# Kernel tuning notes

Hardware: AMD Instinct MI355X
Metric: run time of the kernel (lower is better)

The kernel has to match this reference:

```python
import jax, jax.numpy as jnp
import numpy as np

ANG = 5
WS = 8
HEADS = 2
REF = 2  # refPos = [2, 2]
NEG_SLOPE = 0.1
EPS = 1e-5


def _rel_pos_index(ws):
    coords = np.stack(np.meshgrid(np.arange(ws), np.arange(ws), indexing='ij'))  # [2,ws,ws]
    cf = coords.reshape(2, -1)
    rel = (cf[:, :, None] - cf[:, None, :]).transpose(1, 2, 0)  # [N,N,2]
    rel[..., 0] += ws - 1
    rel[..., 1] += ws - 1
    rel[..., 0] *= 2 * ws - 1
    return jnp.asarray(rel.sum(-1))  # [N,N] int

REL_IDX = _rel_pos_index(WS)


def _ln(x, g, b):
    m = jnp.mean(x, -1, keepdims=True)
    v = jnp.var(x, -1, keepdims=True)
    return (x - m) * jax.lax.rsqrt(v + EPS) * g + b


def setup_inputs():
    key = jax.random.key(0)
    ks = jax.random.split(key, 12)
    b, an2, c, h, w = 2, 25, 32, 96, 96
    C = 2 * c
    s = 0.02
    mlp_hidden = int(C * 4.0)
    inp = {}
    inp['global_fea'] = jax.random.normal(ks[0], (b, an2, c, h, w), jnp.float32)
    inp['centra_fea'] = jax.random.normal(ks[1], (b, c, h, w), jnp.float32)
    inp['disparity'] = jax.random.uniform(ks[2], (b, 1, h, w), jnp.float32)
    inp['qkv_w'] = jax.random.normal(ks[3], (3 * C, C), jnp.float32) * s
    inp['qkv_b'] = jnp.zeros((3 * C,), jnp.float32)
    inp['proj_w'] = jax.random.normal(ks[4], (C, C), jnp.float32) * s
    inp['proj_b'] = jnp.zeros((C,), jnp.float32)
    inp['rpb_table'] = jax.random.normal(ks[5], ((2 * WS - 1) ** 2, HEADS), jnp.float32) * s
    inp['ln1_g'] = jnp.ones((C,), jnp.float32)
    inp['ln1_b'] = jnp.zeros((C,), jnp.float32)
    inp['ln2_g'] = jnp.ones((C,), jnp.float32)
    inp['ln2_b'] = jnp.zeros((C,), jnp.float32)
    inp['fc1_w'] = jax.random.normal(ks[6], (mlp_hidden, C), jnp.float32) * s
    inp['fc1_b'] = jnp.zeros((mlp_hidden,), jnp.float32)
    inp['fc2_w'] = jax.random.normal(ks[7], (C, mlp_hidden), jnp.float32) * s
    inp['fc2_b'] = jnp.zeros((C,), jnp.float32)
    inp['conv_w'] = jax.random.normal(ks[8], (c, C), jnp.float32) * s  # 1x1 conv kernel squeezed
    inp['conv_b'] = jnp.zeros((c,), jnp.float32)
    return inp


def _warp(centra_fea, disparity):
    # back-projection: bilinear warp of the central (2,2) view to all ANG*ANG views
    b, c, h, w = centra_fea.shape
    d = disparity[:, 0]  # [b,h,w]
    ys, xs = jnp.meshgrid(jnp.arange(h, dtype=jnp.float32), jnp.arange(w, dtype=jnp.float32), indexing='ij')
    offs = jnp.asarray([[u - REF, v - REF] for u in range(ANG) for v in range(ANG)], jnp.float32)  # [an2,2]
    sy = ys[None, None] + d[:, None] * offs[None, :, 0, None, None]  # [b,an2,h,w]
    sx = xs[None, None] + d[:, None] * offs[None, :, 1, None, None]
    x0f = jnp.floor(sx)
    y0f = jnp.floor(sy)
    wx = sx - x0f
    wy = sy - y0f
    x0 = jnp.clip(x0f.astype(jnp.int32), 0, w - 1)
    x1 = jnp.clip(x0 + 1, 0, w - 1)
    y0 = jnp.clip(y0f.astype(jnp.int32), 0, h - 1)
    y1 = jnp.clip(y0 + 1, 0, h - 1)
    flat = centra_fea.reshape(b, c, h * w)
    an2 = ANG * ANG

    def gather(yi, xi):
        idx = (yi * w + xi).reshape(b, 1, -1)  # [b,1,an2*h*w]
        g = jnp.take_along_axis(flat, jnp.broadcast_to(idx, (b, c, an2 * h * w)), axis=2)
        return g.reshape(b, c, an2, h, w).transpose(0, 2, 1, 3, 4)  # [b,an2,c,h,w]

    wx_ = wx[:, :, None]
    wy_ = wy[:, :, None]
    return ((1 - wy_) * (1 - wx_) * gather(y0, x0) + (1 - wy_) * wx_ * gather(y0, x1)
            + wy_ * (1 - wx_) * gather(y1, x0) + wy_ * wx_ * gather(y1, x1))


def reference(global_fea, centra_fea, disparity, qkv_w, qkv_b, proj_w, proj_b, rpb_table,
              ln1_g, ln1_b, ln2_g, ln2_b, fc1_w, fc1_b, fc2_w, fc2_b, conv_w, conv_b):
    b, an2, c, h, w = global_fea.shape
    warped = _warp(centra_fea, disparity)
    x = jnp.concatenate([global_fea, warped], axis=2)  # [b,an2,2c,h,w]
    C = 2 * c
    B = b * an2
    # 'b an2 c h w -> (b an2) (h w) c'
    x = x.reshape(B, C, h, w).transpose(0, 2, 3, 1).reshape(B, h * w, C)
    # --- Swin transformer block (shift_size=0, iteration_idx=0) ---
    shortcut = x
    xn = _ln(x, ln1_g, ln1_b).reshape(B, h, w, C)
    nh, nw = h // WS, w // WS
    xw = xn.reshape(B, nh, WS, nw, WS, C).transpose(0, 1, 3, 2, 4, 5).reshape(B * nh * nw, WS * WS, C)
    nwins, N = xw.shape[0], WS * WS
    hd = C // HEADS
    qkv = (xw @ qkv_w.T + qkv_b).reshape(nwins, N, 3, HEADS, hd).transpose(2, 0, 3, 1, 4)
    q, k, v = qkv[0], qkv[1], qkv[2]  # [nwins, heads, N, hd]
    scale = hd ** -0.5
    attn = jnp.einsum('whnd,whmd->whnm', q * scale, k)
    bias = rpb_table[REL_IDX].transpose(2, 0, 1)  # [heads,N,N]
    attn = jax.nn.softmax(attn + bias[None], axis=-1)
    out = jnp.einsum('whnm,whmd->whnd', attn, v).transpose(0, 2, 1, 3).reshape(nwins, N, C)
    out = out @ proj_w.T + proj_b
    out = out.reshape(B, nh, nw, WS, WS, C).transpose(0, 1, 3, 2, 4, 5).reshape(B, h * w, C)
    x = shortcut + out
    xm = _ln(x, ln2_g, ln2_b)
    xm = jax.nn.gelu(xm @ fc1_w.T + fc1_b, approximate=False) @ fc2_w.T + fc2_b
    x = x + xm
    # '(b an2) (h w) c -> (b an2) c h w' then 1x1 conv fuse + LeakyReLU(0.1)
    x = x.reshape(B, h, w, C)
    y = jnp.einsum('bhwc,oc->bohw', x, conv_w) + conv_b[None, :, None, None]
    y = jnp.where(y >= 0, y, NEG_SLOPE * y)
    return y.reshape(b, an2, c, h, w)
```

## Files before the change

### kernel.cpp

```cpp
#include <hip/hip_runtime.h>
#include <hip/hip_bf16.h>
#include <math.h>

#define W_    96
#define HW_   9216
#define NWIN_ 144

typedef __attribute__((ext_vector_type(4))) float          f32x4;
typedef __attribute__((ext_vector_type(8))) __bf16         bf16x8;
typedef __attribute__((ext_vector_type(8))) unsigned short u16x8;

#define MFMA(a,b,c) __builtin_amdgcn_mfma_f32_16x16x32_bf16((a),(b),(c),0,0,0)

#define WOFF_QKV  0
#define WOFF_PROJ 12288
#define WOFF_FC1  16384
#define WOFF_FC2  32768
#define WOFF_CONV 49152
#define WOFF_BIAS 51200
#define WTOT      51200
#define BIAS_N    8192
#define POFF_QKVB  0
#define POFF_PROJB 192
#define POFF_FC1B  256
#define POFF_FC2B  512
#define POFF_CONVB 576
#define POFF_RPB   608
#define POFF_LN1G  1058
#define POFF_LN1B  1122
#define POFF_LN2G  1186
#define POFF_LN2B  1250
#define PTOT       1314

__device__ __forceinline__ float ldin(const void* p, long i, int isbf){
    return isbf ? __bfloat162float(((const __hip_bfloat16*)p)[i]) : ((const float*)p)[i];
}
__device__ __forceinline__ bf16x8 ldbf8(const __bf16* w){
    u16x8 u = *(const u16x8*)w;
    return __builtin_bit_cast(bf16x8, u);
}

__device__ __forceinline__ float gelu_f(float v){
    float u = fabsf(v) * 0.70710678f;
    float t = __builtin_amdgcn_rcpf(1.f + 0.47047f*u);
    float p = t*(0.3480242f + t*(-0.0958798f + t*0.7478556f));
    float er = 1.f - p*__expf(-u*u);
    er = copysignf(er, v);
    return 0.5f*v*(1.f + er);
}

__global__ void probe_kernel(const void* ln1g, int* flag){
    if (threadIdx.x == 0){
        unsigned u = *(const unsigned*)ln1g;
        *flag = (u == 0x3F803F80u) ? 1 : 0;
    }
}

__global__ __launch_bounds__(256) void convert_params(
    const int* __restrict__ flag,
    const void* qkvw, const void* qkvb, const void* projw, const void* projb, const void* rpb,
    const void* ln1g, const void* ln1b, const void* ln2g, const void* ln2b,
    const void* fc1w, const void* fc1b, const void* fc2w, const void* fc2b,
    const void* convw, const void* convb,
    __bf16* __restrict__ wbf, float* __restrict__ pf)
{
    const int isbf = *flag;
    int idx = blockIdx.x*256 + threadIdx.x;
    if (idx >= WTOT + PTOT + BIAS_N) return;
    if (idx < WTOT){
        if      (idx < 12288) wbf[WOFF_QKV  + idx]          = (__bf16)ldin(qkvw, idx, isbf);
        else if (idx < 16384) wbf[WOFF_PROJ + (idx-12288)]  = (__bf16)ldin(projw, idx-12288, isbf);
        else if (idx < 32768) wbf[WOFF_FC1  + (idx-16384)]  = (__bf16)ldin(fc1w, idx-16384, isbf);
        else if (idx < 49152) wbf[WOFF_FC2  + (idx-32768)]  = (__bf16)ldin(fc2w, idx-32768, isbf);
        else                  wbf[WOFF_CONV + (idx-49152)]  = (__bf16)ldin(convw, idx-49152, isbf);
    } else if (idx < WTOT + PTOT){
        int p = idx - WTOT;
        if      (p < 192)  pf[POFF_QKVB  + p]        = ldin(qkvb, p, isbf);
        else if (p < 256)  pf[POFF_PROJB + (p-192)]  = ldin(projb, p-192, isbf);
        else if (p < 512)  pf[POFF_FC1B  + (p-256)]  = ldin(fc1b, p-256, isbf);
        else if (p < 576)  pf[POFF_FC2B  + (p-512)]  = ldin(fc2b, p-512, isbf);
        else if (p < 608)  pf[POFF_CONVB + (p-576)]  = ldin(convb, p-576, isbf);
        else if (p < 1058) pf[POFF_RPB   + (p-608)]  = ldin(rpb, p-608, isbf);
        else if (p < 1122) pf[POFF_LN1G  + (p-1058)] = ldin(ln1g, p-1058, isbf);
        else if (p < 1186) pf[POFF_LN1B  + (p-1122)] = ldin(ln1b, p-1122, isbf);
        else if (p < 1250) pf[POFF_LN2G  + (p-1186)] = ldin(ln2g, p-1186, isbf);
        else               pf[POFF_LN2B  + (p-1250)] = ldin(ln2b, p-1250, isbf);
    } else {
        int eb = idx - (WTOT + PTOT);
        int h = eb >> 12, rem = eb & 4095;
        int i = rem >> 6, j = rem & 63;
        int di = (i>>3)-(j>>3)+7, dj = (i&7)-(j&7)+7;
        wbf[WOFF_BIAS + eb] = (__bf16)ldin(rpb, (di*15+dj)*2 + h, isbf);
    }
}

template<typename T>
__device__ __forceinline__ void phaseA0(
    const T* gf, const T* disp,
    float* tile, int* iy0,int* iy1,int* ix0,int* ix1,float* fys,float* fxs,
    int tid,int b,int a,int wy,int wx,int hw00)
{
    if (tid < 64){
        int ty = tid >> 3, tx = tid & 7;
        int y = wy*8 + ty, x = wx*8 + tx;
        int pix = y*W_ + x;
        float d = (float)disp[(long)b*HW_ + pix];
        float dy = (float)(a/5 - 2), dx = (float)(a%5 - 2);
        float sy = (float)y + d*dy, sx = (float)x + d*dx;
        float y0f = floorf(sy), x0f = floorf(sx);
        fys[tid] = sy - y0f; fxs[tid] = sx - x0f;
        int y0 = min(max((int)y0f,0), W_-1);
        int x0 = min(max((int)x0f,0), W_-1);
        iy0[tid]=y0; iy1[tid]=min(y0+1,W_-1);
        ix0[tid]=x0; ix1[tid]=min(x0+1,W_-1);
    }
    int p = tid & 63;
    long pixoff = hw00 + (p>>3)*W_ + (p&7);
    for (int c = tid>>6; c < 32; c += 4)
        tile[c*67 + p] = (float)gf[(((long)b*25 + a)*32 + c)*HW_ + pixoff];
}

template<typename T>
__device__ __forceinline__ void phaseA1(
    const T* cf, float* tile2,
    const int* iy0,const int* iy1,const int* ix0,const int* ix1,const float* fys,const float* fxs,
    int tid,int b)
{
    int p = tid & 63;
    float fy = fys[p], fx = fxs[p];
    float w00=(1.f-fy)*(1.f-fx), w01=(1.f-fy)*fx, w10=fy*(1.f-fx), w11=fy*fx;
    long r0 = (long)iy0[p]*W_, r1 = (long)iy1[p]*W_;
    int xa = ix0[p], xb = ix1[p];
    for (int c = tid>>6; c < 32; c += 4){
        long cb = ((long)b*32 + c)*HW_;
        float v00 = (float)cf[cb+r0+xa], v01 = (float)cf[cb+r0+xb];
        float v10 = (float)cf[cb+r1+xa], v11 = (float)cf[cb+r1+xb];
        tile2[c*67 + p] = w00*v00 + w01*v01 + w10*v10 + w11*v11;
    }
}

__global__ __launch_bounds__(256) void fused_kernel(
    const int* __restrict__ flag,
    const void* __restrict__ gf, const void* __restrict__ cf, const void* __restrict__ disp,
    const __bf16* __restrict__ wbf, const float* __restrict__ pf,
    void* __restrict__ out)
{
    __shared__ __bf16 xs[64*72];
    __shared__ __bf16 arena[14336];

    const int isbf = *flag;
    const int tid  = threadIdx.x;
    const int lane = tid & 63, wid = tid >> 6;
    const int g = lane >> 4, cl = lane & 15;
    const int bid  = blockIdx.x;
    const int blk  = (bid & 7)*900 + (bid >> 3);
    const int Bidx = blk / NWIN_;
    const int wrem = blk % NWIN_;
    const int wy = wrem / 12, wx = wrem % 12;
    const int b = Bidx / 25, a = Bidx % 25;
    const int hw00 = (wy*8)*W_ + wx*8;

    __bf16* qb  = arena;
    __bf16* kb  = arena + 4608;
    __bf16* vT  = arena + 9216;
    __bf16* xn  = arena + 9728;

    float* tile  = (float*)arena;
    float* tile2 = tile + 2144;
    int*   iy0 = (int*)((char*)arena + 17408);
    int*   iy1 = iy0 + 64;
    int*   ix0 = iy1 + 64;
    int*   ix1 = ix0 + 64;
    float* fys = (float*)(ix1 + 64);
    float* fxs = fys + 64;

    if (isbf) phaseA0((const __hip_bfloat16*)gf, (const __hip_bfloat16*)disp,
                      tile, iy0,iy1,ix0,ix1,fys,fxs, tid,b,a,wy,wx,hw00);
    else      phaseA0((const float*)gf, (const float*)disp,
                      tile, iy0,iy1,ix0,ix1,fys,fxs, tid,b,a,wy,wx,hw00);
    __syncthreads();
    if (isbf) phaseA1((const __hip_bfloat16*)cf, tile2, iy0,iy1,ix0,ix1,fys,fxs, tid,b);
    else      phaseA1((const float*)cf, tile2, iy0,iy1,ix0,ix1,fys,fxs, tid,b);
    __syncthreads();

    {
        const int t = tid>>2, quad = tid&3;
        float v[16]; float sum=0.f, sq=0.f;
        #pragma unroll
        for (int j=0;j<16;++j){
            int c = quad*16+j;
            float val = (c<32) ? tile[c*67 + t] : tile2[(c-32)*67 + t];
            v[j]=val; sum+=val; sq+=val*val;
        }
        sum += __shfl_xor(sum,1); sq += __shfl_xor(sq,1);
        sum += __shfl_xor(sum,2); sq += __shfl_xor(sq,2);
        float m  = sum*(1.f/64.f);
        float rs = rsqrtf(sq*(1.f/64.f) - m*m + 1e-5f);
        bf16x8 s0,s1,n0,n1;
        #pragma unroll
        for (int j=0;j<8;++j){
            int c0 = quad*16+j, c1 = quad*16+8+j;
            s0[j] = (__bf16)v[j];
            s1[j] = (__bf16)v[8+j];
            n0[j] = (__bf16)((v[j]  -m)*rs*pf[POFF_LN1G+c0] + pf[POFF_LN1B+c0]);
            n1[j] = (__bf16)((v[8+j]-m)*rs*pf[POFF_LN1G+c1] + pf[POFF_LN1B+c1]);
        }
        *(bf16x8*)(xs + t*72 + quad*16)     = s0;
        *(bf16x8*)(xs + t*72 + quad*16 + 8) = s1;
        *(bf16x8*)(xn + t*72 + quad*16)     = n0;
        *(bf16x8*)(xn + t*72 + quad*16 + 8) = n1;
    }
    __syncthreads();

    {
        bf16x8 af[4][2];
        #pragma unroll
        for (int m=0;m<4;++m)
            #pragma unroll
            for (int ks=0;ks<2;++ks)
                af[m][ks] = *(const bf16x8*)(xn + (16*m+cl)*72 + ks*32 + 8*g);
        __syncthreads();
        f32x4 acc[3][4];
        #pragma unroll
        for (int nt=0;nt<3;++nt)
            #pragma unroll
            for (int m=0;m<4;++m) acc[nt][m] = (f32x4){0.f,0.f,0.f,0.f};
        const int f = wid*16 + cl;
        #pragma unroll
        for (int ks=0;ks<2;++ks)
            #pragma unroll
            for (int nt=0;nt<3;++nt){
                bf16x8 bw = ldbf8(wbf + WOFF_QKV + (long)(nt*64 + f)*64 + ks*32 + 8*g);
                #pragma unroll
                for (int m=0;m<4;++m) acc[nt][m] = MFMA(af[m][ks], bw, acc[nt][m]);
            }
        float bq = pf[POFF_QKVB + f], bk2 = pf[POFF_QKVB + 64 + f], bv2 = pf[POFF_QKVB + 128 + f];
        #pragma unroll
        for (int m=0;m<4;++m)
            #pragma unroll
            for (int r=0;r<4;++r){
                int t = 16*m + 4*g + r;
                qb[t*72 + f] = (__bf16)((acc[0][m][r] + bq)*0.1767766953f);
                kb[t*72 + f] = (__bf16)(acc[1][m][r] + bk2);
                vT[f*72 + t] = (__bf16)(acc[2][m][r] + bv2);
            }
    }
    __syncthreads();

    const int strip = wid*16;
    f32x4 sc[2][4];
    {
        bf16x8 aq0 = *(const bf16x8*)(qb + (strip+cl)*72 + 8*g);
        bf16x8 aq1 = *(const bf16x8*)(qb + (strip+cl)*72 + 32 + 8*g);
        #pragma unroll
        for (int h=0;h<2;++h)
            #pragma unroll
            for (int jt=0;jt<4;++jt){
                bf16x8 bk = *(const bf16x8*)(kb + (jt*16+cl)*72 + 32*h + 8*g);
                f32x4 z = {0.f,0.f,0.f,0.f};
                sc[h][jt] = MFMA(h?aq1:aq0, bk, z);
            }
        const __bf16* bptr = wbf + WOFF_BIAS + (strip + 4*g)*64 + cl;
        #pragma unroll
        for (int h=0;h<2;++h)
            #pragma unroll
            for (int jt=0;jt<4;++jt)
                #pragma unroll
                for (int r=0;r<4;++r)
                    sc[h][jt][r] += (float)bptr[h*4096 + r*64 + jt*16];
    }
    __syncthreads();

    __bf16* pbuf = qb;
    __bf16* ob   = kb;
    #pragma unroll
    for (int h=0;h<2;++h){
        float inv[4];
        #pragma unroll
        for (int r=0;r<4;++r){
            float m0 = fmaxf(fmaxf(sc[h][0][r],sc[h][1][r]),fmaxf(sc[h][2][r],sc[h][3][r]));
            m0 = fmaxf(m0,__shfl_xor(m0,1));
            m0 = fmaxf(m0,__shfl_xor(m0,2));
            m0 = fmaxf(m0,__shfl_xor(m0,4));
            m0 = fmaxf(m0,__shfl_xor(m0,8));
            float s=0.f;
            #pragma unroll
            for (int jt=0;jt<4;++jt){ float e=__expf(sc[h][jt][r]-m0); sc[h][jt][r]=e; s+=e; }
            s += __shfl_xor(s,1); s += __shfl_xor(s,2);
            s += __shfl_xor(s,4); s += __shfl_xor(s,8);
            inv[r] = 1.f/s;
        }
        #pragma unroll
        for (int jt=0;jt<4;++jt)
            #pragma unroll
            for (int r=0;r<4;++r)
                pbuf[(strip+4*g+r)*72 + jt*16+cl] = (__bf16)(sc[h][jt][r]*inv[r]);
        bf16x8 ap0 = *(const bf16x8*)(pbuf + (strip+cl)*72 + 8*g);
        bf16x8 ap1 = *(const bf16x8*)(pbuf + (strip+cl)*72 + 32 + 8*g);
        f32x4 ov[2];
        ov[0] = (f32x4){0.f,0.f,0.f,0.f};
        ov[1] = (f32x4){0.f,0.f,0.f,0.f};
        #pragma unroll
        for (int ks=0;ks<2;++ks)
            #pragma unroll
            for (int dt=0;dt<2;++dt){
                bf16x8 bv = *(const bf16x8*)(vT + (32*h + dt*16 + cl)*72 + ks*32 + 8*g);
                ov[dt] = MFMA(ks?ap1:ap0, bv, ov[dt]);
            }
        #pragma unroll
        for (int dt=0;dt<2;++dt)
            #pragma unroll
            for (int r=0;r<4;++r)
                ob[(strip+4*g+r)*72 + 32*h + dt*16 + cl] = (__bf16)(ov[dt][r]);
    }
    __syncthreads();

    {
        const int f = wid*16 + cl;
        f32x4 pacc[4];
        #pragma unroll
        for (int m=0;m<4;++m) pacc[m] = (f32x4){0.f,0.f,0.f,0.f};
        #pragma unroll
        for (int ks=0;ks<2;++ks){
            bf16x8 bw = ldbf8(wbf + WOFF_PROJ + (long)f*64 + ks*32 + 8*g);
            #pragma unroll
            for (int m=0;m<4;++m){
                bf16x8 ao = *(const bf16x8*)(ob + (16*m+cl)*72 + ks*32 + 8*g);
                pacc[m] = MFMA(ao, bw, pacc[m]);
            }
        }
        float pbias = pf[POFF_PROJB + f];
        #pragma unroll
        for (int m=0;m<4;++m)
            #pragma unroll
            for (int r=0;r<4;++r){
                int t = 16*m + 4*g + r;
                float y = (float)xs[t*72 + f] + pacc[m][r] + pbias;
                xs[t*72 + f] = (__bf16)y;
            }
    }
    __syncthreads();

    __bf16* xn2 = arena + 9728;
    {
        const int t = tid>>2, quad = tid&3;
        bf16x8 r0 = *(const bf16x8*)(xs + t*72 + quad*16);
        bf16x8 r1 = *(const bf16x8*)(xs + t*72 + quad*16 + 8);
        float v[16]; float sum=0.f, sq=0.f;
        #pragma unroll
        for (int j=0;j<8;++j){ v[j] = (float)r0[j]; v[8+j] = (float)r1[j]; }
        #pragma unroll
        for (int j=0;j<16;++j){ sum += v[j]; sq += v[j]*v[j]; }
        sum += __shfl_xor(sum,1); sq += __shfl_xor(sq,1);
        sum += __shfl_xor(sum,2); sq += __shfl_xor(sq,2);
        float m  = sum*(1.f/64.f);
        float rs = rsqrtf(sq*(1.f/64.f) - m*m + 1e-5f);
        bf16x8 n0,n1;
        #pragma unroll
        for (int j=0;j<8;++j){
            int c0 = quad*16+j, c1 = quad*16+8+j;
            n0[j] = (__bf16)((v[j]  -m)*rs*pf[POFF_LN2G+c0] + pf[POFF_LN2B+c0]);
            n1[j] = (__bf16)((v[8+j]-m)*rs*pf[POFF_LN2G+c1] + pf[POFF_LN2B+c1]);
        }
        *(bf16x8*)(xn2 + t*72 + quad*16)     = n0;
        *(bf16x8*)(xn2 + t*72 + quad*16 + 8) = n1;
    }
    __syncthreads();

    __bf16* hb = arena;
    {
        bf16x8 af[4][2];
        #pragma unroll
        for (int m=0;m<4;++m)
            #pragma unroll
            for (int ks=0;ks<2;++ks)
                af[m][ks] = *(const bf16x8*)(xn2 + (16*m+cl)*72 + ks*32 + 8*g);
        const int f = wid*16 + cl;
        f32x4 acc2[4];
        #pragma unroll
        for (int m=0;m<4;++m) acc2[m] = (f32x4){0.f,0.f,0.f,0.f};
        #pragma unroll
        for (int half=0; half<2; ++half){
            f32x4 a1[2][4];
            #pragma unroll
            for (int nt=0;nt<2;++nt)
                #pragma unroll
                for (int m=0;m<4;++m) a1[nt][m] = (f32x4){0.f,0.f,0.f,0.f};
            #pragma unroll
            for (int ks=0;ks<2;++ks)
                #pragma unroll
                for (int nt=0;nt<2;++nt){
                    int hrow = half*128 + (2*wid+nt)*16 + cl;
                    bf16x8 bw = ldbf8(wbf + WOFF_FC1 + (long)hrow*64 + ks*32 + 8*g);
                    #pragma unroll
                    for (int m=0;m<4;++m) a1[nt][m] = MFMA(af[m][ks], bw, a1[nt][m]);
                }
            #pragma unroll
            for (int nt=0;nt<2;++nt){
                int hrow = half*128 + (2*wid+nt)*16 + cl;
                float hbias = pf[POFF_FC1B + hrow];
                #pragma unroll
                for (int m=0;m<4;++m)
                    #pragma unroll
                    for (int r=0;r<4;++r){
                        float vv = gelu_f(a1[nt][m][r] + hbias);
                        hb[(16*m+4*g+r)*136 + (2*wid+nt)*16 + cl] = (__bf16)vv;
                    }
            }
            __syncthreads();
            #pragma unroll
            for (int ks=0;ks<4;++ks){
                bf16x8 bw = ldbf8(wbf + WOFF_FC2 + (long)f*256 + half*128 + ks*32 + 8*g);
                #pragma unroll
                for (int m=0;m<4;++m){
                    bf16x8 ah = *(const bf16x8*)(hb + (16*m+cl)*136 + ks*32 + 8*g);
                    acc2[m] = MFMA(ah, bw, acc2[m]);
                }
            }
            __syncthreads();
        }
        float b2 = pf[POFF_FC2B + f];
        #pragma unroll
        for (int m=0;m<4;++m)
            #pragma unroll
            for (int r=0;r<4;++r){
                int t = 16*m + 4*g + r;
                float y = (float)xs[t*72 + f] + acc2[m][r] + b2;
                xs[t*72 + f] = (__bf16)y;
            }
    }
    __syncthreads();

    {
        const int nt = wid & 1, mh = wid >> 1;
        f32x4 ca[2];
        ca[0] = (f32x4){0.f,0.f,0.f,0.f};
        ca[1] = (f32x4){0.f,0.f,0.f,0.f};
        #pragma unroll
        for (int ks=0;ks<2;++ks){
            bf16x8 bw = ldbf8(wbf + WOFF_CONV + (long)(nt*16+cl)*64 + ks*32 + 8*g);
            #pragma unroll
            for (int mm=0;mm<2;++mm){
                bf16x8 afr = *(const bf16x8*)(xs + (16*(mh*2+mm)+cl)*72 + ks*32 + 8*g);
                ca[mm] = MFMA(afr, bw, ca[mm]);
            }
        }
        float cbias = pf[POFF_CONVB + nt*16 + cl];
        float* outs = (float*)arena;
        #pragma unroll
        for (int mm=0;mm<2;++mm)
            #pragma unroll
            for (int r=0;r<4;++r){
                int t = 16*(mh*2+mm) + 4*g + r;
                float vv = ca[mm][r] + cbias;
                vv = (vv >= 0.f) ? vv : 0.1f*vv;
                outs[(nt*16+cl)*68 + t] = vv;
            }
    }
    __syncthreads();

    {
        const int co = tid >> 3, seg = tid & 7;
        const float* outs = (const float*)arena;
        long obase = ((long)Bidx*32 + co)*HW_ + hw00 + (long)seg*W_;
        if (isbf){
            bf16x8 vb;
            #pragma unroll
            for (int j=0;j<8;++j) vb[j] = (__bf16)outs[co*68 + seg*8 + j];
            *(bf16x8*)((__hip_bfloat16*)out + obase) = vb;
        } else {
            f32x4 va, vb2;
            #pragma unroll
            for (int j=0;j<4;++j){ va[j] = outs[co*68 + seg*8 + j]; vb2[j] = outs[co*68 + seg*8 + 4 + j]; }
            *(f32x4*)((float*)out + obase)     = va;
            *(f32x4*)((float*)out + obase + 4) = vb2;
        }
    }
}

extern "C" void kernel_launch(void* const* d_in, const int* in_sizes, int n_in,
                              void* d_out, int out_size, void* d_ws, size_t ws_size,
                              hipStream_t stream)
{
    const void* gf    = d_in[0];
    const void* cf    = d_in[1];
    const void* disp  = d_in[2];
    const void* qkvw  = d_in[3];
    const void* qkvb  = d_in[4];
    const void* projw = d_in[5];
    const void* projb = d_in[6];
    const void* rpb   = d_in[7];
    const void* ln1g  = d_in[8];
    const void* ln1b  = d_in[9];
    const void* ln2g  = d_in[10];
    const void* ln2b  = d_in[11];
    const void* fc1w  = d_in[12];
    const void* fc1b  = d_in[13];
    const void* fc2w  = d_in[14];
    const void* fc2b  = d_in[15];
    const void* convw = d_in[16];
    const void* convb = d_in[17];

    int*    flag = (int*)d_ws;
    float*  pf   = (float*)((char*)d_ws + 512);
    __bf16* wbf  = (__bf16*)((char*)d_ws + 8192);

    probe_kernel<<<1, 64, 0, stream>>>(ln1g, flag);

    const int cgrid = (WTOT + PTOT + BIAS_N + 255)/256;
    convert_params<<<cgrid,256,0,stream>>>(flag,
        qkvw,qkvb,projw,projb,rpb,ln1g,ln1b,ln2g,ln2b,
        fc1w,fc1b,fc2w,fc2b,convw,convb, wbf, pf);

    fused_kernel<<<7200,256,0,stream>>>(flag, gf, cf, disp, wbf, pf, d_out);
}
```

Baseline: 390.8 us.

## Merge warp phases, prefetch QKV weights, vectorize bias loads, defer softmax normalization

Merges the two warp phases into one so each thread computes its own bilinear coordinates, which removes the shared-memory index arrays and one barrier. QKV weight fragments are loaded before the gather so their latency can overlap it. The relative-position bias table is permuted into the MFMA register layout so each lane reads it with four 16-byte loads instead of many scalar loads. Softmax normalization moves after the PV MFMA, GELU changes from an erf approximation to a tanh-form sigmoid approximation, and launch bounds now request 4 blocks per CU, which may raise register pressure and changes GELU numerics slightly.

```diff
diff --git a/kernel.cpp b/kernel.cpp
--- a/kernel.cpp
+++ b/kernel.cpp
@@ -41,12 +41,10 @@
 }
 
 __device__ __forceinline__ float gelu_f(float v){
-    float u = fabsf(v) * 0.70710678f;
-    float t = __builtin_amdgcn_rcpf(1.f + 0.47047f*u);
-    float p = t*(0.3480242f + t*(-0.0958798f + t*0.7478556f));
-    float er = 1.f - p*__expf(-u*u);
-    er = copysignf(er, v);
-    return 0.5f*v*(1.f + er);
+    float t = v*v;
+    float w = v*(1.f + 0.044715f*t);
+    float z = __expf(fminf(1.5957691f*w, 80.f));
+    return v*z*__builtin_amdgcn_rcpf(z + 1.f);
 }
 
 __global__ void probe_kernel(const void* ln1g, int* flag){
@@ -87,59 +85,46 @@
         else               pf[POFF_LN2B  + (p-1250)] = ldin(ln2b, p-1250, isbf);
     } else {
         int eb = idx - (WTOT + PTOT);
-        int h = eb >> 12, rem = eb & 4095;
-        int i = rem >> 6, j = rem & 63;
+        int jt = eb & 3, r = (eb>>2)&3, h = (eb>>4)&1, cl = (eb>>5)&15, g = (eb>>9)&3, w = (eb>>11)&3;
+        int i = w*16 + g*4 + r;
+        int j = jt*16 + cl;
         int di = (i>>3)-(j>>3)+7, dj = (i&7)-(j&7)+7;
         wbf[WOFF_BIAS + eb] = (__bf16)ldin(rpb, (di*15+dj)*2 + h, isbf);
     }
 }
 
 template<typename T>
-__device__ __forceinline__ void phaseA0(
-    const T* gf, const T* disp,
-    float* tile, int* iy0,int* iy1,int* ix0,int* ix1,float* fys,float* fxs,
+__device__ __forceinline__ void phaseA(
+    const T* __restrict__ gf, const T* __restrict__ cf, const T* __restrict__ disp,
+    float* tile, float* tile2,
     int tid,int b,int a,int wy,int wx,int hw00)
 {
-    if (tid < 64){
-        int ty = tid >> 3, tx = tid & 7;
-        int y = wy*8 + ty, x = wx*8 + tx;
-        int pix = y*W_ + x;
-        float d = (float)disp[(long)b*HW_ + pix];
-        float dy = (float)(a/5 - 2), dx = (float)(a%5 - 2);
-        float sy = (float)y + d*dy, sx = (float)x + d*dx;
-        float y0f = floorf(sy), x0f = floorf(sx);
-        fys[tid] = sy - y0f; fxs[tid] = sx - x0f;
-        int y0 = min(max((int)y0f,0), W_-1);
-        int x0 = min(max((int)x0f,0), W_-1);
-        iy0[tid]=y0; iy1[tid]=min(y0+1,W_-1);
-        ix0[tid]=x0; ix1[tid]=min(x0+1,W_-1);
-    }
-    int p = tid & 63;
-    long pixoff = hw00 + (p>>3)*W_ + (p&7);
-    for (int c = tid>>6; c < 32; c += 4)
-        tile[c*67 + p] = (float)gf[(((long)b*25 + a)*32 + c)*HW_ + pixoff];
-}
-
-template<typename T>
-__device__ __forceinline__ void phaseA1(
-    const T* cf, float* tile2,
-    const int* iy0,const int* iy1,const int* ix0,const int* ix1,const float* fys,const float* fxs,
-    int tid,int b)
-{
-    int p = tid & 63;
-    float fy = fys[p], fx = fxs[p];
+    const int p = tid & 63;
+    const int ty = p >> 3, tx = p & 7;
+    const int y = wy*8 + ty, x = wx*8 + tx;
+    float d = (float)disp[(long)b*HW_ + y*W_ + x];
+    float dy = (float)(a/5 - 2), dxs = (float)(a%5 - 2);
+    float sy = (float)y + d*dy, sx = (float)x + d*dxs;
+    float y0f = floorf(sy), x0f = floorf(sx);
+    float fy = sy - y0f, fx = sx - x0f;
+    int y0 = min(max((int)y0f,0), W_-1);
+    int x0 = min(max((int)x0f,0), W_-1);
+    int y1 = min(y0+1,W_-1), x1 = min(x0+1,W_-1);
     float w00=(1.f-fy)*(1.f-fx), w01=(1.f-fy)*fx, w10=fy*(1.f-fx), w11=fy*fx;
-    long r0 = (long)iy0[p]*W_, r1 = (long)iy1[p]*W_;
-    int xa = ix0[p], xb = ix1[p];
-    for (int c = tid>>6; c < 32; c += 4){
-        long cb = ((long)b*32 + c)*HW_;
-        float v00 = (float)cf[cb+r0+xa], v01 = (float)cf[cb+r0+xb];
-        float v10 = (float)cf[cb+r1+xa], v11 = (float)cf[cb+r1+xb];
+    long r0 = (long)y0*W_, r1 = (long)y1*W_;
+    const int c0 = tid>>6;
+    long gbase = (((long)b*25 + a)*32 + c0)*HW_ + hw00 + ty*W_ + tx;
+    long cbase = ((long)b*32 + c0)*HW_;
+    for (int c = c0; c < 32; c += 4){
+        tile[c*67 + p] = (float)gf[gbase];
+        float v00 = (float)cf[cbase+r0+x0], v01 = (float)cf[cbase+r0+x1];
+        float v10 = (float)cf[cbase+r1+x0], v11 = (float)cf[cbase+r1+x1];
         tile2[c*67 + p] = w00*v00 + w01*v01 + w10*v10 + w11*v11;
-    }
-}
-
-__global__ __launch_bounds__(256) void fused_kernel(
+        gbase += 4*HW_; cbase += 4*HW_;
+    }
+}
+
+__global__ __launch_bounds__(256,4) void fused_kernel(
     const int* __restrict__ flag,
     const void* __restrict__ gf, const void* __restrict__ cf, const void* __restrict__ disp,
     const __bf16* __restrict__ wbf, const float* __restrict__ pf,
@@ -159,6 +144,7 @@
     const int wy = wrem / 12, wx = wrem % 12;
     const int b = Bidx / 25, a = Bidx % 25;
     const int hw00 = (wy*8)*W_ + wx*8;
+    const int f = wid*16 + cl;
 
     __bf16* qb  = arena;
     __bf16* kb  = arena + 4608;
@@ -167,20 +153,18 @@
 
     float* tile  = (float*)arena;
     float* tile2 = tile + 2144;
-    int*   iy0 = (int*)((char*)arena + 17408);
-    int*   iy1 = iy0 + 64;
-    int*   ix0 = iy1 + 64;
-    int*   ix1 = ix0 + 64;
-    float* fys = (float*)(ix1 + 64);
-    float* fxs = fys + 64;
-
-    if (isbf) phaseA0((const __hip_bfloat16*)gf, (const __hip_bfloat16*)disp,
-                      tile, iy0,iy1,ix0,ix1,fys,fxs, tid,b,a,wy,wx,hw00);
-    else      phaseA0((const float*)gf, (const float*)disp,
-                      tile, iy0,iy1,ix0,ix1,fys,fxs, tid,b,a,wy,wx,hw00);
-    __syncthreads();
-    if (isbf) phaseA1((const __hip_bfloat16*)cf, tile2, iy0,iy1,ix0,ix1,fys,fxs, tid,b);
-    else      phaseA1((const float*)cf, tile2, iy0,iy1,ix0,ix1,fys,fxs, tid,b);
+
+    bf16x8 wq[3][2];
+    #pragma unroll
+    for (int nt=0;nt<3;++nt)
+        #pragma unroll
+        for (int ks=0;ks<2;++ks)
+            wq[nt][ks] = ldbf8(wbf + WOFF_QKV + (long)(nt*64 + f)*64 + ks*32 + 8*g);
+
+    if (isbf) phaseA((const __hip_bfloat16*)gf, (const __hip_bfloat16*)cf,
+                     (const __hip_bfloat16*)disp, tile, tile2, tid,b,a,wy,wx,hw00);
+    else      phaseA((const float*)gf, (const float*)cf,
+                     (const float*)disp, tile, tile2, tid,b,a,wy,wx,hw00);
     __syncthreads();
 
     {
@@ -225,15 +209,12 @@
         for (int nt=0;nt<3;++nt)
             #pragma unroll
             for (int m=0;m<4;++m) acc[nt][m] = (f32x4){0.f,0.f,0.f,0.f};
-        const int f = wid*16 + cl;
         #pragma unroll
         for (int ks=0;ks<2;++ks)
             #pragma unroll
-            for (int nt=0;nt<3;++nt){
-                bf16x8 bw = ldbf8(wbf + WOFF_QKV + (long)(nt*64 + f)*64 + ks*32 + 8*g);
+            for (int nt=0;nt<3;++nt)
                 #pragma unroll
-                for (int m=0;m<4;++m) acc[nt][m] = MFMA(af[m][ks], bw, acc[nt][m]);
-            }
+                for (int m=0;m<4;++m) acc[nt][m] = MFMA(af[m][ks], wq[nt][ks], acc[nt][m]);
         float bq = pf[POFF_QKVB + f], bk2 = pf[POFF_QKVB + 64 + f], bv2 = pf[POFF_QKVB + 128 + f];
         #pragma unroll
         for (int m=0;m<4;++m)
@@ -260,14 +241,19 @@
                 f32x4 z = {0.f,0.f,0.f,0.f};
                 sc[h][jt] = MFMA(h?aq1:aq0, bk, z);
             }
-        const __bf16* bptr = wbf + WOFF_BIAS + (strip + 4*g)*64 + cl;
+        const __bf16* bbase = wbf + WOFF_BIAS + ((wid*4+g)*16+cl)*32;
+        bf16x8 bch[4];
+        #pragma unroll
+        for (int q2=0;q2<4;++q2) bch[q2] = ldbf8(bbase + q2*8);
         #pragma unroll
         for (int h=0;h<2;++h)
             #pragma unroll
-            for (int jt=0;jt<4;++jt)
+            for (int r=0;r<4;++r)
                 #pragma unroll
-                for (int r=0;r<4;++r)
-                    sc[h][jt][r] += (float)bptr[h*4096 + r*64 + jt*16];
+                for (int jt=0;jt<4;++jt){
+                    int e = h*16 + r*4 + jt;
+                    sc[h][jt][r] += (float)bch[e>>3][e&7];
+                }
     }
     __syncthreads();
 
@@ -294,7 +280,7 @@
         for (int jt=0;jt<4;++jt)
             #pragma unroll
             for (int r=0;r<4;++r)
-                pbuf[(strip+4*g+r)*72 + jt*16+cl] = (__bf16)(sc[h][jt][r]*inv[r]);
+                pbuf[(strip+4*g+r)*72 + jt*16+cl] = (__bf16)sc[h][jt][r];
         bf16x8 ap0 = *(const bf16x8*)(pbuf + (strip+cl)*72 + 8*g);
         bf16x8 ap1 = *(const bf16x8*)(pbuf + (strip+cl)*72 + 32 + 8*g);
         f32x4 ov[2];
@@ -311,12 +297,11 @@
         for (int dt=0;dt<2;++dt)
             #pragma unroll
             for (int r=0;r<4;++r)
-                ob[(strip+4*g+r)*72 + 32*h + dt*16 + cl] = (__bf16)(ov[dt][r]);
-    }
-    __syncthreads();
-
-    {
-        const int f = wid*16 + cl;
+                ob[(strip+4*g+r)*72 + 32*h + dt*16 + cl] = (__bf16)(ov[dt][r]*inv[r]);
+    }
+    __syncthreads();
+
+    {
         f32x4 pacc[4];
         #pragma unroll
         for (int m=0;m<4;++m) pacc[m] = (f32x4){0.f,0.f,0.f,0.f};
@@ -375,7 +360,6 @@
             #pragma unroll
             for (int ks=0;ks<2;++ks)
                 af[m][ks] = *(const bf16x8*)(xn2 + (16*m+cl)*72 + ks*32 + 8*g);
-        const int f = wid*16 + cl;
         f32x4 acc2[4];
         #pragma unroll
         for (int m=0;m<4;++m) acc2[m] = (f32x4){0.f,0.f,0.f,0.f};
```

After: 338.1 us. 1.16x faster.
